# Performance work log

Hardware: AMD Instinct MI355X
Metric: run time of the kernel (lower is better)

The kernel has to match this reference:

```python
import jax, jax.numpy as jnp
import numpy as np

EMBED_DIM = 768
NUM_HEADS = 12


def setup_inputs() -> dict:
    key = jax.random.key(0)
    ks = jax.random.split(key, 9)
    C = EMBED_DIM
    x = jax.random.normal(ks[0], (8, 3136, C), dtype=jnp.float32)
    s = 0.02
    Wq = jax.random.normal(ks[1], (C, C), dtype=jnp.float32) * s
    Wk = jax.random.normal(ks[2], (C, C), dtype=jnp.float32) * s
    Wv = jax.random.normal(ks[3], (C, C), dtype=jnp.float32) * s
    Wo = jax.random.normal(ks[4], (C, C), dtype=jnp.float32) * s
    bq = jax.random.normal(ks[5], (C,), dtype=jnp.float32) * s
    bk = jax.random.normal(ks[6], (C,), dtype=jnp.float32) * s
    bv = jax.random.normal(ks[7], (C,), dtype=jnp.float32) * s
    bo = jax.random.normal(ks[8], (C,), dtype=jnp.float32) * s
    return {"x": x, "Wq": Wq, "bq": bq, "Wk": Wk, "bk": bk,
            "Wv": Wv, "bv": bv, "Wo": Wo, "bo": bo, "T": 16}


def reference(x, Wq, bq, Wk, bk, Wv, bv, Wo, bo, T):
    B, N, C = x.shape
    H = NUM_HEADS
    hd = C // H
    Hh = H // 2
    P = N // T
    scale = 1.0 / np.sqrt(hd).astype(np.float32)

    Q = (x @ Wq + bq).reshape(B, T, P, H, hd)
    K = (x @ Wk + bk).reshape(B, T, P, H, hd)
    V = (x @ Wv + bv).reshape(B, T, P, H, hd)

    # spatial attention: first Hh heads, attend over patches within each frame
    Qs, Ks, Vs = Q[..., :Hh, :], K[..., :Hh, :], V[..., :Hh, :]
    scores_s = jnp.einsum('btphd,btqhd->bthpq', Qs, Ks) * scale  # (B,T,Hh,P,P)
    ws = jax.nn.softmax(scores_s, axis=-1)
    out_s = jnp.einsum('bthpq,btqhd->btphd', ws, Vs)  # (B,T,P,Hh,hd)

    # temporal attention: last Hh heads, attend over frames at each patch
    Qt, Kt, Vt = Q[..., Hh:, :], K[..., Hh:, :], V[..., Hh:, :]
    scores_t = jnp.einsum('btphd,bsphd->bphts', Qt, Kt) * scale  # (B,P,Hh,T,T)
    wt = jax.nn.softmax(scores_t, axis=-1)
    out_t = jnp.einsum('bphts,bsphd->btphd', wt, Vt)  # (B,T,P,Hh,hd)

    out = jnp.concatenate([out_s, out_t], axis=3).reshape(B, N, C)
    return out @ Wo + bo
```

## Files before the change

kernel.cpp:

```cpp
#include <hip/hip_runtime.h>


typedef __attribute__((ext_vector_type(8))) short short8;
typedef __attribute__((ext_vector_type(4))) float f32x4;

typedef __attribute__((address_space(1))) void gvoid;
typedef __attribute__((address_space(3))) void lvoid;

__device__ __forceinline__ unsigned short f2b(float f) {
  unsigned int u = __float_as_uint(f);
  unsigned int r = (u + 0x7FFFu + ((u >> 16) & 1u)) >> 16;
  return (unsigned short)r;
}

__global__ __launch_bounds__(256) void k_prep(
    const float* __restrict__ x, unsigned short* __restrict__ xb,
    const float* __restrict__ bq, const float* __restrict__ bk,
    const float* __restrict__ bv, float* __restrict__ bqkv,
    const float* __restrict__ Wq, const float* __restrict__ Wk,
    const float* __restrict__ Wv, const float* __restrict__ Wo,
    unsigned short* __restrict__ wqkvT, unsigned short* __restrict__ woT) {
  __shared__ float tile[32][33];
  if (blockIdx.x < 18816) {
    int tid = blockIdx.x * 256 + threadIdx.x;
    if (tid < 2304)
      bqkv[tid] = tid < 768 ? bq[tid] : (tid < 1536 ? bk[tid - 768] : bv[tid - 1536]);
    float4 v = ((const float4*)x)[tid];
    ushort4 o;
    o.x = f2b(v.x); o.y = f2b(v.y); o.z = f2b(v.z); o.w = f2b(v.w);
    ((ushort4*)xb)[tid] = o;
    return;
  }
  int bid = blockIdx.x - 18816;
  const float* W;
  unsigned short* dst;
  int n0, k0;
  if (bid < 1728) {
    int tn = bid % 72, tk = bid / 72;
    n0 = tn * 32; k0 = tk * 32;
    int which = n0 / 768;
    W = which == 0 ? Wq : (which == 1 ? Wk : Wv);
    dst = wqkvT;
  } else {
    int b2 = bid - 1728;
    int tn = b2 % 24, tk = b2 / 24;
    n0 = tn * 32; k0 = tk * 32;
    W = Wo; dst = woT;
  }
  int nn0 = n0 % 768;
  for (int i = threadIdx.x; i < 1024; i += 256) {
    int r = i >> 5, c = i & 31;
    tile[r][c] = W[(size_t)(k0 + r) * 768 + nn0 + c];
  }
  __syncthreads();
  for (int i = threadIdx.x; i < 1024; i += 256) {
    int r = i >> 5, c = i & 31;
    dst[(size_t)(n0 + r) * 768 + k0 + c] = f2b(tile[c][r]);
  }
}


#define FENCE asm volatile("" ::: "memory")
#define BARRIER do { FENCE; __builtin_amdgcn_s_barrier(); FENCE; } while (0)
#define WAIT_LGKM0 asm volatile("s_waitcnt lgkmcnt(0)" ::: "memory")
#define WAIT_VM4 asm volatile("s_waitcnt vmcnt(4)" ::: "memory")

#define STAGE(PBASE, BUFBASE, HT, KT_) do {                                          \
    int kt__ = (KT_);                                                                \
    bool real__ = (kt__ < 12);                                                       \
    if (!real__) kt__ -= 12;                                                         \
    const unsigned short* src__ = (PBASE) + (HT) * 98304 + kt__ * 64;                \
    unsigned d0__ = real__ ? ((BUFBASE) + (HT) * 8192 + w * 512) : (65536u + w * 512); \
    unsigned d1__ = real__ ? ((BUFBASE) + (HT) * 8192 + 4096 + w * 512) : (65536u + w * 512); \
    __builtin_amdgcn_global_load_lds((const gvoid*)src__, (lvoid*)(lds + d0__), 16, 0, 0); \
    __builtin_amdgcn_global_load_lds((const gvoid*)(src__ + 49152), (lvoid*)(lds + d1__), 16, 0, 0); \
  } while (0)

#define LDA(MH, ABASE) do {                                                          \
    const unsigned short* ab__ = lds + (ABASE) + ((MH) * 128 + arow) * 64;           \
    _Pragma("unroll")                                                                \
    for (int mf = 0; mf < 4; ++mf) {                                                 \
      af[mf][0] = *(const short8*)(ab__ + mf * 1024 + s0);                           \
      af[mf][1] = *(const short8*)(ab__ + mf * 1024 + s1);                           \
    }                                                                                \
  } while (0)

#define LDB(NH, BBASE) do {                                                          \
    const unsigned short* bb__ = lds + (BBASE) + ((NH) * 128 + brow) * 64;           \
    _Pragma("unroll")                                                                \
    for (int nf = 0; nf < 2; ++nf) {                                                 \
      bf[nf][0] = *(const short8*)(bb__ + nf * 1024 + s0);                           \
      bf[nf][1] = *(const short8*)(bb__ + nf * 1024 + s1);                           \
    }                                                                                \
  } while (0)

#define MM(MH, NH) do {                                                              \
    __builtin_amdgcn_s_setprio(1);                                                   \
    _Pragma("unroll")                                                                \
    for (int mf = 0; mf < 4; ++mf) {                                                 \
      _Pragma("unroll")                                                              \
      for (int nf = 0; nf < 2; ++nf) {                                               \
        acc[MH][mf][NH][nf] = __builtin_amdgcn_mfma_f32_16x16x32_bf16(               \
            af[mf][0], bf[nf][0], acc[MH][mf][NH][nf], 0, 0, 0);                     \
        acc[MH][mf][NH][nf] = __builtin_amdgcn_mfma_f32_16x16x32_bf16(               \
            af[mf][1], bf[nf][1], acc[MH][mf][NH][nf], 0, 0, 0);                     \
      }                                                                              \
    }                                                                                \
    __builtin_amdgcn_s_setprio(0);                                                   \
  } while (0)

__global__ __launch_bounds__(512, 2) void k_gemm256(
    const unsigned short* __restrict__ A, const unsigned short* __restrict__ Bt,
    const float* __restrict__ bias, unsigned short* __restrict__ Cout,
    int M, int N) {
  __shared__ __align__(16) unsigned short lds[69632];
  const int nwg = gridDim.x;
  const int nbx = N >> 8;
  const int orig = blockIdx.x;
  const int q = nwg >> 3, r = nwg & 7;
  const int xcd = orig & 7, lin = orig >> 3;
  const int wg = (xcd < r ? xcd * (q + 1) : r * (q + 1) + (xcd - r) * q) + lin;
  const int m0 = (wg / nbx) << 8, n0 = (wg % nbx) << 8;

  const int tid = threadIdx.x;
  const int w = tid >> 6, l = tid & 63;
  const int wm = w >> 2, wn = w & 3;
  const int lg = l >> 4, ln = l & 15;
  const int arow = wm * 64 + ln;
  const int brow = wn * 32 + ln;
  const int s0 = (lg ^ (ln & 7)) * 8;
  const int s1 = s0 ^ 32;
  const int srow = tid >> 3;
  const int slg8 = ((tid & 7) ^ (srow & 7)) * 8;
  const unsigned short* pA = A + (size_t)(m0 + srow) * 768 + slg8;
  const unsigned short* pB = Bt + (size_t)(n0 + srow) * 768 + slg8;

  f32x4 acc[2][4][2][2] = {};

  STAGE(pA, 0,     0, 0);
  STAGE(pB, 16384, 0, 0);
  STAGE(pA, 0,     1, 0);
  STAGE(pB, 16384, 1, 0);
  STAGE(pA, 32768, 0, 1);
  STAGE(pB, 49152, 1, 1);
  WAIT_VM4;
  BARRIER;

  for (int it = 0; it < 6; ++it) {
    const int kt1 = 2 * it + 1, ktn0 = 2 * it + 2, ktn1 = 2 * it + 3;
    short8 af[4][2], bf[2][2];
    LDA(0, 0); LDB(0, 16384);
    STAGE(pA, 32768, 1, kt1);
    BARRIER; WAIT_LGKM0; MM(0, 0);
    LDB(1, 16384);
    STAGE(pB, 49152, 0, kt1);
    BARRIER; WAIT_LGKM0; MM(0, 1);
    LDA(1, 0);
    STAGE(pA, 0, 0, ktn0);
    BARRIER; WAIT_LGKM0; MM(1, 1);
    LDB(0, 16384);
    STAGE(pB, 16384, 1, ktn0);
    WAIT_VM4;
    BARRIER; WAIT_LGKM0; MM(1, 0);
    LDA(0, 32768); LDB(0, 49152);
    STAGE(pA, 0, 1, ktn0);
    BARRIER; WAIT_LGKM0; MM(0, 0);
    LDB(1, 49152);
    STAGE(pB, 16384, 0, ktn0);
    BARRIER; WAIT_LGKM0; MM(0, 1);
    LDA(1, 32768);
    STAGE(pA, 32768, 0, ktn1);
    BARRIER; WAIT_LGKM0; MM(1, 1);
    LDB(0, 49152);
    STAGE(pB, 49152, 1, ktn1);
    WAIT_VM4;
    BARRIER; WAIT_LGKM0; MM(1, 0);
  }

#pragma unroll
  for (int mh = 0; mh < 2; ++mh)
#pragma unroll
    for (int mf = 0; mf < 4; ++mf)
#pragma unroll
      for (int nh = 0; nh < 2; ++nh)
#pragma unroll
        for (int nf = 0; nf < 2; ++nf) {
          const int col = n0 + nh * 128 + wn * 32 + nf * 16 + ln;
          const float bval = bias[col];
          const int row = m0 + mh * 128 + wm * 64 + mf * 16 + lg * 4;
#pragma unroll
          for (int rr = 0; rr < 4; ++rr)
            Cout[(size_t)(row + rr) * N + col] = f2b(acc[mh][mf][nh][nf][rr] + bval);
        }
}

__global__ __launch_bounds__(256) void k_gemm_out(
    const unsigned short* __restrict__ A, const unsigned short* __restrict__ Bt,
    const float* __restrict__ bias, float* __restrict__ C,
    int M, int N, int K) {
  __shared__ __align__(16) unsigned short lds[26624];
  const int tid = threadIdx.x;
  const int w = tid >> 6, l = tid & 63;
  const int lg = l >> 4, ln = l & 15;
  const int m0 = blockIdx.y * 128, n0 = blockIdx.x * 128;
  const int wr = (w >> 1) * 64, wc = (w & 1) * 64;
  f32x4 acc[4][4] = {};
  const int srow = tid >> 2;
  const int sg = ((tid & 3) ^ (srow & 3)) * 8;
  const unsigned short* ga = A + (size_t)(m0 + srow) * K + sg;
  const unsigned short* gb = Bt + (size_t)(n0 + srow) * K + sg;
  const size_t krow64 = (size_t)64 * K;
  const int wofs = w * 512;
  const int rs = (lg ^ (ln & 3)) * 8;

#define OSTAGE3(BUF, K0, REAL) do {                                                                \
    int k__ = (REAL) ? (K0) : 0;                                                                   \
    unsigned a__ = (REAL) ? ((unsigned)(BUF) * 8192u + wofs) : (24576u + wofs);                    \
    unsigned b__ = (REAL) ? ((unsigned)(BUF) * 8192u + 4096u + wofs) : (24576u + wofs);            \
    __builtin_amdgcn_global_load_lds((const gvoid*)(ga + k__),          (lvoid*)(lds + a__),        16, 0, 0); \
    __builtin_amdgcn_global_load_lds((const gvoid*)(ga + krow64 + k__), (lvoid*)(lds + a__ + 2048), 16, 0, 0); \
    __builtin_amdgcn_global_load_lds((const gvoid*)(gb + k__),          (lvoid*)(lds + b__),        16, 0, 0); \
    __builtin_amdgcn_global_load_lds((const gvoid*)(gb + krow64 + k__), (lvoid*)(lds + b__ + 2048), 16, 0, 0); \
  } while (0)

  OSTAGE3(0, 0, true);
  OSTAGE3(1, 32, true);
  WAIT_VM4;
  BARRIER;
  int bcur = 0, bnxt = 1, bpre = 2;
  const int nk = K >> 5;
  for (int i = 0; i < nk; ++i) {
    OSTAGE3(bpre, (i + 2) * 32, i + 2 < nk);
    const unsigned short* as = lds + bcur * 8192;
    const unsigned short* bs = as + 4096;
    short8 a[4], b[4];
#pragma unroll
    for (int mt = 0; mt < 4; ++mt)
      a[mt] = *(const short8*)(as + (wr + mt * 16 + ln) * 32 + rs);
#pragma unroll
    for (int nt = 0; nt < 4; ++nt)
      b[nt] = *(const short8*)(bs + (wc + nt * 16 + ln) * 32 + rs);
#pragma unroll
    for (int mt = 0; mt < 4; ++mt)
#pragma unroll
      for (int nt = 0; nt < 4; ++nt)
        acc[mt][nt] = __builtin_amdgcn_mfma_f32_16x16x32_bf16(a[mt], b[nt], acc[mt][nt], 0, 0, 0);
    WAIT_VM4;
    BARRIER;
    int t = bcur; bcur = bnxt; bnxt = bpre; bpre = t;
  }
#pragma unroll
  for (int nt = 0; nt < 4; ++nt) {
    int col = n0 + wc + nt * 16 + ln;
    float bval = bias[col];
#pragma unroll
    for (int mt = 0; mt < 4; ++mt) {
      int row = m0 + wr + mt * 16 + lg * 4;
#pragma unroll
      for (int r = 0; r < 4; ++r)
        C[(size_t)(row + r) * N + col] = acc[mt][nt][r] + bval;
    }
  }
#undef OSTAGE3
}

__global__ __launch_bounds__(256) void k_attn_fused(
    const unsigned short* __restrict__ qkv, unsigned short* __restrict__ attn) {
  __shared__ __align__(16) unsigned short smem[29696];
  const int w = threadIdx.x >> 6, l = threadIdx.x & 63;
  const int lg = l >> 4, ln = l & 15;
  const float scale = 0.125f;
  if (blockIdx.x < 768) {
    const int bi = blockIdx.x;
    const int h = bi % 6;
    const int t = (bi / 6) % 16;
    const int b = bi / 96;
    const int base_row = b * 3136 + t * 196;
    unsigned short* Vt = smem;
    unsigned short* Pl = smem + 14848;
    for (int i = threadIdx.x; i < 196 * 8; i += 256) {
      int key = i >> 3, d0 = (i & 7) * 8;
      short8 v = *(const short8*)(qkv + (size_t)(base_row + key) * 2304 + 1536 + h * 64 + d0);
#pragma unroll
      for (int j = 0; j < 8; ++j) Vt[(d0 + j) * 232 + key] = (unsigned short)v[j];
    }
    for (int i = threadIdx.x; i < 64 * 28; i += 256)
      Vt[(i / 28) * 232 + 196 + (i % 28)] = 0;
    __syncthreads();
    for (int mt = w; mt < 13; mt += 4) {
      int qm = mt * 16 + ln; if (qm > 195) qm = 195;
      const size_t qoff = (size_t)(base_row + qm) * 2304 + h * 64 + lg * 8;
      short8 qa0 = *(const short8*)(qkv + qoff);
      short8 qa1 = *(const short8*)(qkv + qoff + 32);
      f32x4 st[13];
#pragma unroll
      for (int nt = 0; nt < 13; ++nt) {
        int kn = nt * 16 + ln; if (kn > 195) kn = 195;
        const size_t koff = (size_t)(base_row + kn) * 2304 + 768 + h * 64 + lg * 8;
        short8 kb0 = *(const short8*)(qkv + koff);
        short8 kb1 = *(const short8*)(qkv + koff + 32);
        f32x4 s = {0.f, 0.f, 0.f, 0.f};
        s = __builtin_amdgcn_mfma_f32_16x16x32_bf16(qa0, kb0, s, 0, 0, 0);
        s = __builtin_amdgcn_mfma_f32_16x16x32_bf16(qa1, kb1, s, 0, 0, 0);
        st[nt] = s;
      }
      float mr[4] = {-1e30f, -1e30f, -1e30f, -1e30f};
#pragma unroll
      for (int nt = 0; nt < 13; ++nt) {
        bool valid = (nt * 16 + ln) < 196;
#pragma unroll
        for (int r = 0; r < 4; ++r) {
          float v = valid ? st[nt][r] * scale : -1e30f;
          st[nt][r] = v;
          mr[r] = fmaxf(mr[r], v);
        }
      }
#pragma unroll
      for (int msk = 1; msk <= 8; msk <<= 1)
#pragma unroll
        for (int r = 0; r < 4; ++r) mr[r] = fmaxf(mr[r], __shfl_xor(mr[r], msk));
      float sm[4] = {0.f, 0.f, 0.f, 0.f};
#pragma unroll
      for (int nt = 0; nt < 13; ++nt)
#pragma unroll
        for (int r = 0; r < 4; ++r) {
          float p = __expf(st[nt][r] - mr[r]);
          st[nt][r] = p;
          sm[r] += p;
        }
#pragma unroll
      for (int msk = 1; msk <= 8; msk <<= 1)
#pragma unroll
        for (int r = 0; r < 4; ++r) sm[r] += __shfl_xor(sm[r], msk);
      float inv[4];
#pragma unroll
      for (int r = 0; r < 4; ++r) inv[r] = 1.f / sm[r];
      unsigned short* Pw = Pl + w * 16 * 232;
#pragma unroll
      for (int nt = 0; nt < 13; ++nt)
#pragma unroll
        for (int r = 0; r < 4; ++r)
          Pw[(lg * 4 + r) * 232 + nt * 16 + ln] = f2b(st[nt][r] * inv[r]);
#pragma unroll
      for (int r = 0; r < 4; ++r) Pw[ln * 232 + 208 + lg * 4 + r] = 0;
#pragma unroll
      for (int nt4 = 0; nt4 < 4; ++nt4) {
        f32x4 acc = {0.f, 0.f, 0.f, 0.f};
#pragma unroll
        for (int ks = 0; ks < 7; ++ks) {
          short8 pa = *(const short8*)(Pw + ln * 232 + ks * 32 + lg * 8);
          short8 vb = *(const short8*)(Vt + (nt4 * 16 + ln) * 232 + ks * 32 + lg * 8);
          acc = __builtin_amdgcn_mfma_f32_16x16x32_bf16(pa, vb, acc, 0, 0, 0);
        }
#pragma unroll
        for (int r = 0; r < 4; ++r) {
          int m = mt * 16 + lg * 4 + r;
          if (m < 196)
            attn[(size_t)(base_row + m) * 768 + h * 64 + nt4 * 16 + ln] = f2b(acc[r]);
        }
      }
    }
  } else {
    const int u = (blockIdx.x - 768) * 4 + w;
    const int b = u / 1176;
    const int rem = u % 1176;
    const int p = rem / 6;
    const int h = 6 + rem % 6;
    const size_t rowb = (size_t)b * 3136 + p;
    unsigned short* Vt = smem + w * 2560;
    unsigned short* Pl = smem + 10240 + w * 640;
    for (int i = l; i < 128; i += 64) {
      int tt = i >> 3, d0 = (i & 7) * 8;
      short8 v = *(const short8*)(qkv + (rowb + (size_t)tt * 196) * 2304 + 1536 + h * 64 + d0);
#pragma unroll
      for (int j = 0; j < 8; ++j) Vt[(d0 + j) * 40 + tt] = (unsigned short)v[j];
    }
    for (int i = l; i < 1024; i += 64)
      Vt[(i >> 4) * 40 + 16 + (i & 15)] = 0;
    const size_t qoff = (rowb + (size_t)ln * 196) * 2304 + h * 64 + lg * 8;
    short8 qa0 = *(const short8*)(qkv + qoff);
    short8 qa1 = *(const short8*)(qkv + qoff + 32);
    short8 kb0 = *(const short8*)(qkv + qoff + 768);
    short8 kb1 = *(const short8*)(qkv + qoff + 768 + 32);
    f32x4 s = {0.f, 0.f, 0.f, 0.f};
    s = __builtin_amdgcn_mfma_f32_16x16x32_bf16(qa0, kb0, s, 0, 0, 0);
    s = __builtin_amdgcn_mfma_f32_16x16x32_bf16(qa1, kb1, s, 0, 0, 0);
    float stv[4], mr[4];
#pragma unroll
    for (int r = 0; r < 4; ++r) { stv[r] = s[r] * scale; mr[r] = stv[r]; }
#pragma unroll
    for (int msk = 1; msk <= 8; msk <<= 1)
#pragma unroll
      for (int r = 0; r < 4; ++r) mr[r] = fmaxf(mr[r], __shfl_xor(mr[r], msk));
    float sm[4];
#pragma unroll
    for (int r = 0; r < 4; ++r) { stv[r] = __expf(stv[r] - mr[r]); sm[r] = stv[r]; }
#pragma unroll
    for (int msk = 1; msk <= 8; msk <<= 1)
#pragma unroll
      for (int r = 0; r < 4; ++r) sm[r] += __shfl_xor(sm[r], msk);
#pragma unroll
    for (int r = 0; r < 4; ++r)
      Pl[(lg * 4 + r) * 40 + ln] = f2b(stv[r] / sm[r]);
#pragma unroll
    for (int r = 0; r < 4; ++r) Pl[ln * 40 + 16 + lg * 4 + r] = 0;
    short8 pa = *(const short8*)(Pl + ln * 40 + lg * 8);
#pragma unroll
    for (int nt4 = 0; nt4 < 4; ++nt4) {
      short8 vb = *(const short8*)(Vt + (nt4 * 16 + ln) * 40 + lg * 8);
      f32x4 acc = {0.f, 0.f, 0.f, 0.f};
      acc = __builtin_amdgcn_mfma_f32_16x16x32_bf16(pa, vb, acc, 0, 0, 0);
#pragma unroll
      for (int r = 0; r < 4; ++r) {
        int tq = lg * 4 + r;
        attn[((size_t)b * 3136 + (size_t)tq * 196 + p) * 768 + h * 64 + nt4 * 16 + ln] = f2b(acc[r]);
      }
    }
  }
}

extern "C" void kernel_launch(void* const* d_in, const int* in_sizes, int n_in,
                              void* d_out, int out_size, void* d_ws, size_t ws_size,
                              hipStream_t stream) {
  const float* x  = (const float*)d_in[0];
  const float* Wq = (const float*)d_in[1];
  const float* bq = (const float*)d_in[2];
  const float* Wk = (const float*)d_in[3];
  const float* bk = (const float*)d_in[4];
  const float* Wv = (const float*)d_in[5];
  const float* bv = (const float*)d_in[6];
  const float* Wo = (const float*)d_in[7];
  const float* bo = (const float*)d_in[8];
  float* out = (float*)d_out;
  char* ws = (char*)d_ws;
  unsigned short* xb    = (unsigned short*)(ws + 0);
  unsigned short* wqkvT = (unsigned short*)(ws + 38535168);
  float*          bqkv  = (float*)(ws + 42074112);
  unsigned short* woT   = (unsigned short*)(ws + 42083328);
  unsigned short* qkvb  = (unsigned short*)(ws + 43262976);
  unsigned short* attnb = (unsigned short*)(ws + 158868480);

  k_prep<<<21120, 256, 0, stream>>>(x, xb, bq, bk, bv, bqkv, Wq, Wk, Wv, Wo, wqkvT, woT);
  k_gemm256<<<882, 512, 0, stream>>>(xb, wqkvT, bqkv, qkvb, 25088, 2304);
  k_attn_fused<<<3120, 256, 0, stream>>>(qkvb, attnb);
  k_gemm_out<<<dim3(6, 196), 256, 0, stream>>>(attnb, woT, bo, out, 25088, 768, 768);
}
```

Baseline: 247.4 us.

## Widen output GEMM tile to 128x192 with double-buffered LDS staging

```diff
diff --git a/kernel.cpp b/kernel.cpp
--- a/kernel.cpp
+++ b/kernel.cpp
@@ -194,63 +194,61 @@
         }
 }
 
-__global__ __launch_bounds__(256) void k_gemm_out(
+__global__ __launch_bounds__(256, 3) void k_gemm_out(
     const unsigned short* __restrict__ A, const unsigned short* __restrict__ Bt,
     const float* __restrict__ bias, float* __restrict__ C,
     int M, int N, int K) {
-  __shared__ __align__(16) unsigned short lds[26624];
+  __shared__ __align__(16) unsigned short lds[22528];
   const int tid = threadIdx.x;
   const int w = tid >> 6, l = tid & 63;
   const int lg = l >> 4, ln = l & 15;
-  const int m0 = blockIdx.y * 128, n0 = blockIdx.x * 128;
-  const int wr = (w >> 1) * 64, wc = (w & 1) * 64;
-  f32x4 acc[4][4] = {};
+  const int m0 = blockIdx.y * 128, n0 = blockIdx.x * 192;
+  const int wr = (w >> 1) * 64, wc = (w & 1) * 96;
+  f32x4 acc[4][6] = {};
   const int srow = tid >> 2;
   const int sg = ((tid & 3) ^ (srow & 3)) * 8;
   const unsigned short* ga = A + (size_t)(m0 + srow) * K + sg;
   const unsigned short* gb = Bt + (size_t)(n0 + srow) * K + sg;
-  const size_t krow64 = (size_t)64 * K;
   const int wofs = w * 512;
   const int rs = (lg ^ (ln & 3)) * 8;
 
-#define OSTAGE3(BUF, K0, REAL) do {                                                                \
-    int k__ = (REAL) ? (K0) : 0;                                                                   \
-    unsigned a__ = (REAL) ? ((unsigned)(BUF) * 8192u + wofs) : (24576u + wofs);                    \
-    unsigned b__ = (REAL) ? ((unsigned)(BUF) * 8192u + 4096u + wofs) : (24576u + wofs);            \
-    __builtin_amdgcn_global_load_lds((const gvoid*)(ga + k__),          (lvoid*)(lds + a__),        16, 0, 0); \
-    __builtin_amdgcn_global_load_lds((const gvoid*)(ga + krow64 + k__), (lvoid*)(lds + a__ + 2048), 16, 0, 0); \
-    __builtin_amdgcn_global_load_lds((const gvoid*)(gb + k__),          (lvoid*)(lds + b__),        16, 0, 0); \
-    __builtin_amdgcn_global_load_lds((const gvoid*)(gb + krow64 + k__), (lvoid*)(lds + b__ + 2048), 16, 0, 0); \
+#define OSTAGE(BUF, K0) do {                                                                       \
+    const unsigned base__ = (unsigned)(BUF) * 10240u;                                              \
+    _Pragma("unroll")                                                                              \
+    for (int j = 0; j < 2; ++j)                                                                    \
+      __builtin_amdgcn_global_load_lds((const gvoid*)(ga + (size_t)(j * 64) * K + (K0)),           \
+                                       (lvoid*)(lds + base__ + j * 2048 + wofs), 16, 0, 0);        \
+    _Pragma("unroll")                                                                              \
+    for (int j = 0; j < 3; ++j)                                                                    \
+      __builtin_amdgcn_global_load_lds((const gvoid*)(gb + (size_t)(j * 64) * K + (K0)),           \
+                                       (lvoid*)(lds + base__ + 4096 + j * 2048 + wofs), 16, 0, 0); \
   } while (0)
 
-  OSTAGE3(0, 0, true);
-  OSTAGE3(1, 32, true);
-  WAIT_VM4;
+  OSTAGE(0, 0);
+  asm volatile("s_waitcnt vmcnt(0)" ::: "memory");
   BARRIER;
-  int bcur = 0, bnxt = 1, bpre = 2;
   const int nk = K >> 5;
   for (int i = 0; i < nk; ++i) {
-    OSTAGE3(bpre, (i + 2) * 32, i + 2 < nk);
-    const unsigned short* as = lds + bcur * 8192;
+    if (i + 1 < nk) OSTAGE((i + 1) & 1, (i + 1) * 32);
+    const unsigned short* as = lds + (i & 1) * 10240;
     const unsigned short* bs = as + 4096;
-    short8 a[4], b[4];
+    short8 a[4], b[6];
 #pragma unroll
     for (int mt = 0; mt < 4; ++mt)
       a[mt] = *(const short8*)(as + (wr + mt * 16 + ln) * 32 + rs);
 #pragma unroll
-    for (int nt = 0; nt < 4; ++nt)
+    for (int nt = 0; nt < 6; ++nt)
       b[nt] = *(const short8*)(bs + (wc + nt * 16 + ln) * 32 + rs);
 #pragma unroll
     for (int mt = 0; mt < 4; ++mt)
 #pragma unroll
-      for (int nt = 0; nt < 4; ++nt)
+      for (int nt = 0; nt < 6; ++nt)
         acc[mt][nt] = __builtin_amdgcn_mfma_f32_16x16x32_bf16(a[mt], b[nt], acc[mt][nt], 0, 0, 0);
-    WAIT_VM4;
+    asm volatile("s_waitcnt vmcnt(0)" ::: "memory");
     BARRIER;
-    int t = bcur; bcur = bnxt; bnxt = bpre; bpre = t;
-  }
-#pragma unroll
-  for (int nt = 0; nt < 4; ++nt) {
+  }
+#pragma unroll
+  for (int nt = 0; nt < 6; ++nt) {
     int col = n0 + wc + nt * 16 + ln;
     float bval = bias[col];
 #pragma unroll
@@ -261,7 +259,7 @@
         C[(size_t)(row + r) * N + col] = acc[mt][nt][r] + bval;
     }
   }
-#undef OSTAGE3
+#undef OSTAGE
 }
 
 __global__ __launch_bounds__(256) void k_attn_fused(
@@ -443,5 +441,5 @@
   k_prep<<<21120, 256, 0, stream>>>(x, xb, bq, bk, bv, bqkv, Wq, Wk, Wv, Wo, wqkvT, woT);
   k_gemm256<<<882, 512, 0, stream>>>(xb, wqkvT, bqkv, qkvb, 25088, 2304);
   k_attn_fused<<<3120, 256, 0, stream>>>(qkvb, attnb);
-  k_gemm_out<<<dim3(6, 196), 256, 0, stream>>>(attnb, woT, bo, out, 25088, 768, 768);
-}
+  k_gemm_out<<<dim3(4, 196), 256, 0, stream>>>(attnb, woT, bo, out, 25088, 768, 768);
+}
```

New measurement: 244.5 us. No clear change (-1.1%).
